# Performance work log

Hardware: AMD Instinct MI355X
Metric: run time of the kernel (lower is better)

Reference implementation:

```python
import jax, jax.numpy as jnp
import numpy as np

E = 1024
B, QL, KVL = 8, 2048, 2048


def setup_inputs() -> dict:
    key = jax.random.key(0)
    ks = jax.random.split(key, 12)
    s = 1.0 / np.sqrt(E)
    return {
        "query": jax.random.normal(ks[0], (B, QL, E), jnp.float32),
        "key_value": jax.random.normal(ks[1], (B, KVL, E), jnp.float32),
        "attention_mask": jax.random.randint(ks[2], (B, QL, KVL), 0, 2, jnp.int32),
        "Wq": jax.random.uniform(ks[3], (E, E), jnp.float32, -s, s),
        "bq": jax.random.uniform(ks[4], (E,), jnp.float32, -s, s),
        "Wk": jax.random.uniform(ks[5], (E, E), jnp.float32, -s, s),
        "bk": jax.random.uniform(ks[6], (E,), jnp.float32, -s, s),
        "Wv": jax.random.uniform(ks[7], (E, E), jnp.float32, -s, s),
        "bv": jax.random.uniform(ks[8], (E,), jnp.float32, -s, s),
        "Wo": jax.random.uniform(ks[9], (E, E), jnp.float32, -s, s),
        "bo": jax.random.uniform(ks[10], (E,), jnp.float32, -s, s),
    }


def reference(query, key_value, attention_mask, Wq, bq, Wk, bk, Wv, bv, Wo, bo):
    # torch Linear: x @ W.T + b
    q = jnp.einsum('bqe,fe->bqf', query, Wq) + bq          # [B, QL, E]
    k = jnp.einsum('bke,fe->bkf', key_value, Wk) + bk      # [B, KVL, E]
    v = jnp.einsum('bke,fe->bkf', key_value, Wv) + bv      # [B, KVL, E]
    scale = 1.0 / jnp.sqrt(jnp.asarray(q.shape[-1], q.dtype))
    attn = jnp.einsum('bqe,bke->bqk', q, k) * scale        # [B, QL, KVL]
    attn = jnp.where(attention_mask == 0, -jnp.inf, attn)
    attn = jax.nn.softmax(attn, axis=-1)
    out = jnp.einsum('bqk,bke->bqe', attn, v)              # [B, QL, E]
    out = jnp.einsum('bqe,fe->bqf', out, Wo) + bo
    return out
```

## Files before the change

### kernel.cpp

```cpp
#include <hip/hip_runtime.h>
#include <hip/hip_bf16.h>
#include <stdint.h>

typedef unsigned short u16;
typedef short s16x8 __attribute__((ext_vector_type(8)));
typedef u16 u16x8 __attribute__((ext_vector_type(8)));
typedef u16 u16x4 __attribute__((ext_vector_type(4)));
typedef float f32x4 __attribute__((ext_vector_type(4)));

__device__ __forceinline__ u16 f2bf(float f) {
  union { float f; uint32_t u; } c; c.f = f;
  uint32_t u = c.u;
  u = u + 0x7fffu + ((u >> 16) & 1u);
  return (u16)(u >> 16);
}
__device__ __forceinline__ float bf2f(u16 b) {
  union { uint32_t u; float f; } c; c.u = ((uint32_t)b) << 16;
  return c.f;
}

__device__ __forceinline__ void gld_lds16(const u16* g, u16* l) {
  __builtin_amdgcn_global_load_lds(
      (const __attribute__((address_space(1))) uint32_t*)g,
      (__attribute__((address_space(3))) uint32_t*)l,
      16, 0, 0);
}

__global__ __launch_bounds__(256) void cvt_f32_to_bf16(
    const float* __restrict__ in, u16* __restrict__ out, long n8) {
  long i = (long)blockIdx.x * blockDim.x + threadIdx.x;
  if (i >= n8) return;
  const float4 a = ((const float4*)in)[i * 2];
  const float4 b = ((const float4*)in)[i * 2 + 1];
  u16x8 r;
  r[0] = f2bf(a.x); r[1] = f2bf(a.y); r[2] = f2bf(a.z); r[3] = f2bf(a.w);
  r[4] = f2bf(b.x); r[5] = f2bf(b.y); r[6] = f2bf(b.z); r[7] = f2bf(b.w);
  *(u16x8*)&out[i * 8] = r;
}

__global__ __launch_bounds__(256) void cvt_w4(
    const float* __restrict__ w0, const float* __restrict__ w1,
    const float* __restrict__ w2, const float* __restrict__ w3,
    u16* __restrict__ out) {
  const float* src = (blockIdx.y == 0) ? w0 : (blockIdx.y == 1) ? w1
                   : (blockIdx.y == 2) ? w2 : w3;
  const long i = (long)blockIdx.x * blockDim.x + threadIdx.x;
  const float4 a = ((const float4*)src)[i * 2];
  const float4 b = ((const float4*)src)[i * 2 + 1];
  u16x8 r;
  r[0] = f2bf(a.x); r[1] = f2bf(a.y); r[2] = f2bf(a.z); r[3] = f2bf(a.w);
  r[4] = f2bf(b.x); r[5] = f2bf(b.y); r[6] = f2bf(b.z); r[7] = f2bf(b.w);
  *(u16x8*)&out[(long)blockIdx.y * 1048576 + i * 8] = r;
}

__global__ __launch_bounds__(256) void transpose64(
    const u16* __restrict__ in, u16* __restrict__ out, int R, int C) {
  __shared__ u16 t[64][66];
  const long ib = (long)blockIdx.z * (long)R * C;
  const int r0 = blockIdx.x * 64, c0 = blockIdx.y * 64;
  const int tid = threadIdx.x;
#pragma unroll
  for (int i = 0; i < 2; ++i) {
    const int ch = i * 256 + tid;
    const int r = ch >> 3, cc = ch & 7;
    const s16x8 v = *(const s16x8*)&in[ib + (long)(r0 + r) * C + c0 + cc * 8];
#pragma unroll
    for (int j = 0; j < 8; ++j) t[r][cc * 8 + j] = (u16)v[j];
  }
  __syncthreads();
#pragma unroll
  for (int i = 0; i < 2; ++i) {
    const int ch = i * 256 + tid;
    const int c = ch >> 3, rr = ch & 7;
    u16x8 r8;
#pragma unroll
    for (int j = 0; j < 8; ++j) r8[j] = t[rr * 8 + j][c];
    *(u16x8*)&out[ib + (long)(c0 + c) * R + r0 + rr * 8] = r8;
  }
}

__global__ __launch_bounds__(256) void bgemv(
    const u16* __restrict__ matA, const float* __restrict__ vecA,
    const u16* __restrict__ matB, const float* __restrict__ vecB,
    const float* __restrict__ addB, float* __restrict__ outA,
    float* __restrict__ outB, float scaleA) {
  __shared__ float w[1024];
  const int tid = threadIdx.x;
  const bool second = blockIdx.x >= 64;
  const u16* mat = second ? matB : matA;
  const float* vec = second ? vecB : vecA;
  const int rb = (second ? (int)blockIdx.x - 64 : (int)blockIdx.x) * 16;
#pragma unroll
  for (int i = 0; i < 4; ++i) w[i * 256 + tid] = vec[i * 256 + tid];
  __syncthreads();
  const int lane = tid & 63, wv_ = tid >> 6;
#pragma unroll
  for (int r = 0; r < 4; ++r) {
    const int row = rb + wv_ * 4 + r;
    const u16* p = &mat[(long)row * 1024 + lane * 16];
    const u16x8 a = *(const u16x8*)p;
    const u16x8 b = *(const u16x8*)(p + 8);
    float s = 0.f;
#pragma unroll
    for (int j = 0; j < 8; ++j) s += bf2f(a[j]) * w[lane * 16 + j];
#pragma unroll
    for (int j = 0; j < 8; ++j) s += bf2f(b[j]) * w[lane * 16 + 8 + j];
#pragma unroll
    for (int off = 32; off >= 1; off >>= 1) s += __shfl_xor(s, off);
    if (lane == 0) {
      if (second) outB[row] = s + addB[row];
      else        outA[row] = s * scaleA;
    }
  }
}

__global__ __launch_bounds__(256) void cgemv(
    const u16* __restrict__ kvbf, const float* __restrict__ wvec,
    float* __restrict__ c) {
  __shared__ float w[1024];
  const int tid = threadIdx.x;
#pragma unroll
  for (int i = 0; i < 4; ++i) w[i * 256 + tid] = wvec[i * 256 + tid];
  __syncthreads();
  const int lane = tid & 63, wv_ = tid >> 6;
  const long rowbase = (long)blockIdx.x * 16 + wv_ * 4;
#pragma unroll
  for (int r = 0; r < 4; ++r) {
    const long row = rowbase + r;
    const u16* p = &kvbf[row * 1024 + lane * 16];
    const u16x8 a = *(const u16x8*)p;
    const u16x8 b = *(const u16x8*)(p + 8);
    float s = 0.f;
#pragma unroll
    for (int j = 0; j < 8; ++j) s += bf2f(a[j]) * w[lane * 16 + j];
#pragma unroll
    for (int j = 0; j < 8; ++j) s += bf2f(b[j]) * w[lane * 16 + 8 + j];
#pragma unroll
    for (int off = 32; off >= 1; off >>= 1) s += __shfl_xor(s, off);
    if (lane == 0) c[row] = s;
  }
}

__global__ __launch_bounds__(256) void softmax_rows(u16* __restrict__ S) {
  const long base = (long)blockIdx.x * 2048;
  const int tid = threadIdx.x;
  const int lane = tid & 63, wave = tid >> 6;
  u16x8 raw = *(const u16x8*)&S[base + tid * 8];
  float v[8];
#pragma unroll
  for (int j = 0; j < 8; ++j) v[j] = bf2f(raw[j]);
  float m = v[0];
#pragma unroll
  for (int j = 1; j < 8; ++j) m = fmaxf(m, v[j]);
#pragma unroll
  for (int off = 32; off >= 1; off >>= 1) m = fmaxf(m, __shfl_xor(m, off));
  __shared__ float red[8];
  if (lane == 0) red[wave] = m;
  __syncthreads();
  m = fmaxf(fmaxf(red[0], red[1]), fmaxf(red[2], red[3]));
  float s = 0.f;
#pragma unroll
  for (int j = 0; j < 8; ++j) { v[j] = __expf(v[j] - m); s += v[j]; }
#pragma unroll
  for (int off = 32; off >= 1; off >>= 1) s += __shfl_xor(s, off);
  if (lane == 0) red[4 + wave] = s;
  __syncthreads();
  s = (red[4] + red[5]) + (red[6] + red[7]);
  const float inv = 1.f / s;
#pragma unroll
  for (int j = 0; j < 8; ++j) raw[j] = f2bf(v[j] * inv);
  *(u16x8*)&S[base + tid * 8] = raw;
}

union __align__(16) SmemT {
  u16 stage[2][128 * 64];
  float epi[32 * 132];
};

__device__ __forceinline__ s16x8 ldsfrag(const u16* p, int r, int c8) {
  return *(const s16x8*)&p[r * 64 + ((c8 ^ (r & 7)) << 3)];
}

__device__ __forceinline__ void stage128(const u16* __restrict__ gb, int row0,
                                         int K, int k0, u16* lbuf, int tid) {
#pragma unroll
  for (int i = 0; i < 4; ++i) {
    const int f = i * 256 + tid;
    const int rl = f >> 3, s = f & 7;
    const int gc = (s ^ (rl & 7)) << 3;
    gld_lds16(gb + (long)(row0 + rl) * K + k0 + gc, lbuf + f * 8);
  }
}

template<bool HAS_BIAS, int MODE, bool HAS_MASK>
__global__ __launch_bounds__(256, 4) void gemm128(
    const u16* __restrict__ A, const u16* __restrict__ B,
    const float* __restrict__ bias, const int* __restrict__ mask,
    void* __restrict__ Cv,
    int M, int N, int K, long sA, long sB, long sC, long sMask, long sBias,
    float scale) {
  __shared__ SmemT sm;
  const int nx = gridDim.x, ny = gridDim.y;
  const int did = blockIdx.x + nx * (blockIdx.y + ny * blockIdx.z);
  const int cpx = (nx * ny * gridDim.z) >> 3;
  const int nf = (did & 7) * cpx + (did >> 3);
  const int b = nf / (nx * ny);
  const int rr = nf % (nx * ny);
  const int bm = (rr / ny) * 128;
  const int bn = (rr % ny) * 128;

  const u16* Ab = A + (long)b * sA;
  const u16* Bb = B + (long)b * sB;
  const float* biasB = HAS_BIAS ? (bias + (long)b * sBias) : nullptr;
  const int tid = threadIdx.x;
  const int lane = tid & 63, wave = tid >> 6;
  const int wm = wave >> 1, wn = wave & 1;
  const int lr = lane & 15, lk = lane >> 4;
  const int NT = K >> 6;

  f32x4 acc[4][4] = {};

  for (int t = 0; t < NT; ++t) {
    stage128(Ab, bm, K, t << 6, sm.stage[0], tid);
    stage128(Bb, bn, K, t << 6, sm.stage[1], tid);
    asm volatile("s_waitcnt vmcnt(0)" ::: "memory");
    __syncthreads();
#pragma unroll
    for (int ks = 0; ks < 2; ++ks) {
      s16x8 af[4], bg[4];
#pragma unroll
      for (int mi = 0; mi < 4; ++mi)
        af[mi] = ldsfrag(sm.stage[0], wm * 64 + mi * 16 + lr, ks * 4 + lk);
#pragma unroll
      for (int ni = 0; ni < 4; ++ni)
        bg[ni] = ldsfrag(sm.stage[1], wn * 64 + ni * 16 + lr, ks * 4 + lk);
#pragma unroll
      for (int mi = 0; mi < 4; ++mi)
#pragma unroll
        for (int ni = 0; ni < 4; ++ni)
          acc[mi][ni] = __builtin_amdgcn_mfma_f32_16x16x32_bf16(
              af[mi], bg[ni], acc[mi][ni], 0, 0, 0);
    }
    __syncthreads();
  }

  const long cb = (long)b * sC;
  const int q = tid & 7, r = tid >> 3;
#pragma unroll
  for (int h = 0; h < 4; ++h) {
    __syncthreads();
    if (wm == (h >> 1)) {
      const int mi0 = (h & 1) * 2;
#pragma unroll
      for (int mm = 0; mm < 2; ++mm) {
        const int mi = mi0 + mm;
#pragma unroll
        for (int ni = 0; ni < 4; ++ni) {
          const int c = wn * 64 + ni * 16 + lr;
          const float bvx = HAS_BIAS ? biasB[bn + c] : 0.f;
#pragma unroll
          for (int j = 0; j < 4; ++j)
            sm.epi[(mm * 16 + (lk << 2) + j) * 132 + c] =
                acc[mi][ni][j] * scale + bvx;
        }
      }
    }
    __syncthreads();
    const int growi = bm + h * 32 + r;
    const long grow = cb + (long)growi * N + bn;
    const long mrow = HAS_MASK
        ? ((long)b * sMask + (long)growi * (long)N + bn) : 0;
#pragma unroll
    for (int ch = 0; ch < 2; ++ch) {
      const int c0 = ch * 64 + q * 8;
      const float4 x = *(const float4*)&sm.epi[r * 132 + c0];
      const float4 y = *(const float4*)&sm.epi[r * 132 + c0 + 4];
      if (MODE == 1) {
        *(float4*)&((float*)Cv)[grow + c0] = x;
        *(float4*)&((float*)Cv)[grow + c0 + 4] = y;
      } else {
        u16x8 pk;
        if (HAS_MASK) {
          const int4 ma = *(const int4*)&mask[mrow + c0];
          const int4 mb = *(const int4*)&mask[mrow + c0 + 4];
          pk[0] = f2bf(ma.x ? x.x : -1e30f);
          pk[1] = f2bf(ma.y ? x.y : -1e30f);
          pk[2] = f2bf(ma.z ? x.z : -1e30f);
          pk[3] = f2bf(ma.w ? x.w : -1e30f);
          pk[4] = f2bf(mb.x ? y.x : -1e30f);
          pk[5] = f2bf(mb.y ? y.y : -1e30f);
          pk[6] = f2bf(mb.z ? y.z : -1e30f);
          pk[7] = f2bf(mb.w ? y.w : -1e30f);
        } else {
          pk[0] = f2bf(x.x); pk[1] = f2bf(x.y);
          pk[2] = f2bf(x.z); pk[3] = f2bf(x.w);
          pk[4] = f2bf(y.x); pk[5] = f2bf(y.y);
          pk[6] = f2bf(y.z); pk[7] = f2bf(y.w);
        }
        *(u16x8*)&((u16*)Cv)[grow + c0] = pk;
      }
    }
  }
}

extern "C" void kernel_launch(void* const* d_in, const int* in_sizes, int n_in,
                              void* d_out, int out_size, void* d_ws, size_t ws_size,
                              hipStream_t stream) {
  const float* query = (const float*)d_in[0];
  const float* kv    = (const float*)d_in[1];
  const int*   mask  = (const int*)d_in[2];
  const float* Wq = (const float*)d_in[3];
  const float* bq = (const float*)d_in[4];
  const float* Wk = (const float*)d_in[5];
  const float* bk = (const float*)d_in[6];
  const float* Wv = (const float*)d_in[7];
  const float* bv = (const float*)d_in[8];
  const float* Wo = (const float*)d_in[9];
  const float* bo = (const float*)d_in[10];
  float* out = (float*)d_out;
  (void)bk;

  char* ws = (char*)d_ws;
  const size_t MB = (size_t)1 << 20;
  u16* qbf  = (u16*)(ws + 0);
  u16* kvbf = (u16*)(ws + 32 * MB);
  u16* wq   = (u16*)(ws + 64 * MB);
  u16* wo   = (u16*)(ws + 70 * MB);
  u16* WqT  = (u16*)(ws + 72 * MB);
  u16* WkT  = (u16*)(ws + 74 * MB);
  u16* Mt   = (u16*)(ws + 78 * MB);
  u16* Wvo  = (u16*)(ws + 80 * MB);
  float* wvec = (float*)(ws + 82 * MB);
  float* bvo  = (float*)(ws + 82 * MB + 65536);
  float* cvec = (float*)(ws + 83 * MB);
  u16* qM   = (u16*)(ws + 84 * MB);
  u16* VwT  = (u16*)(ws + 116 * MB);
  u16* S    = (u16*)(ws + 148 * MB);

  const long sQK = (long)2048 * 1024;
  const long sS  = (long)2048 * 2048;

  cvt_f32_to_bf16<<<8192, 256, 0, stream>>>(query, qbf, 2097152);
  cvt_f32_to_bf16<<<8192, 256, 0, stream>>>(kv, kvbf, 2097152);
  cvt_w4<<<dim3(512, 4, 1), 256, 0, stream>>>(Wq, Wk, Wv, Wo, wq);
  transpose64<<<dim3(16, 16, 3), 256, 0, stream>>>(wq, WqT, 1024, 1024);
  bgemv<<<128, 256, 0, stream>>>(WkT, bq, wo, bv, bo, wvec, bvo, 0.03125f);
  cgemv<<<1024, 256, 0, stream>>>(kvbf, wvec, cvec);

  gemm128<false, 0, false><<<dim3(8, 8, 2), 256, 0, stream>>>(
      WkT, WqT, nullptr, nullptr, Mt, 1024, 1024, 1024,
      -2097152L, 2097152L, 1048576L, 0, 0, 1.f);

  gemm128<false, 0, false><<<dim3(128, 8, 1), 256, 0, stream>>>(
      qbf, Mt, nullptr, nullptr, qM, 16384, 1024, 1024, 0, 0, 0, 0, 0, 1.f);

  gemm128<false, 0, false><<<dim3(8, 16, 8), 256, 0, stream>>>(
      Wvo, kvbf, nullptr, nullptr, VwT, 1024, 2048, 1024,
      0, sQK, sQK, 0, 0, 1.f);

  gemm128<true, 0, true><<<dim3(16, 16, 8), 256, 0, stream>>>(
      qM, kvbf, cvec, mask, S, 2048, 2048, 1024, sQK, sQK, sS, sS, 2048,
      0.03125f);

  softmax_rows<<<16384, 256, 0, stream>>>(S);

  gemm128<true, 1, false><<<dim3(16, 8, 8), 256, 0, stream>>>(
      S, VwT, bvo, nullptr, out, 2048, 1024, 2048, sS, sQK, sQK, 0, 0, 1.f);
}
```

Baseline: 338.1 us.

## Fuse fp32-to-bf16 conversions into transpose, gemv, and GEMM A-tile staging

Merges weight conversion with transposition into a single kernel, fuses the key/value conversion with the c-vector gemv, and drops the separate query conversion by converting fp32 query tiles inside the GEMM's A staging. This removes several launches and intermediate bf16 round trips through memory. The query GEMM now loads fp32 through registers rather than direct-to-LDS async loads, doubling A-side bytes and possibly hurting that GEMM's throughput.

Measured after the change: 351.7 us. 4.0% more time.

```diff
diff --git a/kernel.cpp b/kernel.cpp
--- a/kernel.cpp
+++ b/kernel.cpp
@@ -26,46 +26,40 @@
       16, 0, 0);
 }
 
-__global__ __launch_bounds__(256) void cvt_f32_to_bf16(
-    const float* __restrict__ in, u16* __restrict__ out, long n8) {
-  long i = (long)blockIdx.x * blockDim.x + threadIdx.x;
-  if (i >= n8) return;
-  const float4 a = ((const float4*)in)[i * 2];
-  const float4 b = ((const float4*)in)[i * 2 + 1];
-  u16x8 r;
-  r[0] = f2bf(a.x); r[1] = f2bf(a.y); r[2] = f2bf(a.z); r[3] = f2bf(a.w);
-  r[4] = f2bf(b.x); r[5] = f2bf(b.y); r[6] = f2bf(b.z); r[7] = f2bf(b.w);
-  *(u16x8*)&out[i * 8] = r;
-}
-
-__global__ __launch_bounds__(256) void cvt_w4(
-    const float* __restrict__ w0, const float* __restrict__ w1,
-    const float* __restrict__ w2, const float* __restrict__ w3,
-    u16* __restrict__ out) {
-  const float* src = (blockIdx.y == 0) ? w0 : (blockIdx.y == 1) ? w1
-                   : (blockIdx.y == 2) ? w2 : w3;
-  const long i = (long)blockIdx.x * blockDim.x + threadIdx.x;
-  const float4 a = ((const float4*)src)[i * 2];
-  const float4 b = ((const float4*)src)[i * 2 + 1];
-  u16x8 r;
-  r[0] = f2bf(a.x); r[1] = f2bf(a.y); r[2] = f2bf(a.z); r[3] = f2bf(a.w);
-  r[4] = f2bf(b.x); r[5] = f2bf(b.y); r[6] = f2bf(b.z); r[7] = f2bf(b.w);
-  *(u16x8*)&out[(long)blockIdx.y * 1048576 + i * 8] = r;
-}
-
-__global__ __launch_bounds__(256) void transpose64(
-    const u16* __restrict__ in, u16* __restrict__ out, int R, int C) {
+__global__ __launch_bounds__(256) void cvt_wt(
+    const float* __restrict__ Wq, const float* __restrict__ Wk,
+    const float* __restrict__ Wv, const float* __restrict__ Wo,
+    u16* __restrict__ WqT, u16* __restrict__ WkT, u16* __restrict__ WvT,
+    u16* __restrict__ wo) {
+  const int z = blockIdx.z;
+  const int tid = threadIdx.x;
+  if (z == 3) {
+    const long base = ((long)(blockIdx.y * 16 + blockIdx.x)) * 4096 + tid * 16;
+#pragma unroll
+    for (int h = 0; h < 2; ++h) {
+      const float4 a = *(const float4*)&Wo[base + h * 8];
+      const float4 b = *(const float4*)&Wo[base + h * 8 + 4];
+      u16x8 r;
+      r[0] = f2bf(a.x); r[1] = f2bf(a.y); r[2] = f2bf(a.z); r[3] = f2bf(a.w);
+      r[4] = f2bf(b.x); r[5] = f2bf(b.y); r[6] = f2bf(b.z); r[7] = f2bf(b.w);
+      *(u16x8*)&wo[base + h * 8] = r;
+    }
+    return;
+  }
+  const float* src = (z == 0) ? Wq : (z == 1) ? Wk : Wv;
+  u16* dst = (z == 0) ? WqT : (z == 1) ? WkT : WvT;
   __shared__ u16 t[64][66];
-  const long ib = (long)blockIdx.z * (long)R * C;
   const int r0 = blockIdx.x * 64, c0 = blockIdx.y * 64;
-  const int tid = threadIdx.x;
 #pragma unroll
   for (int i = 0; i < 2; ++i) {
     const int ch = i * 256 + tid;
     const int r = ch >> 3, cc = ch & 7;
-    const s16x8 v = *(const s16x8*)&in[ib + (long)(r0 + r) * C + c0 + cc * 8];
-#pragma unroll
-    for (int j = 0; j < 8; ++j) t[r][cc * 8 + j] = (u16)v[j];
+    const float4 a = *(const float4*)&src[(long)(r0 + r) * 1024 + c0 + cc * 8];
+    const float4 b = *(const float4*)&src[(long)(r0 + r) * 1024 + c0 + cc * 8 + 4];
+    t[r][cc * 8 + 0] = f2bf(a.x); t[r][cc * 8 + 1] = f2bf(a.y);
+    t[r][cc * 8 + 2] = f2bf(a.z); t[r][cc * 8 + 3] = f2bf(a.w);
+    t[r][cc * 8 + 4] = f2bf(b.x); t[r][cc * 8 + 5] = f2bf(b.y);
+    t[r][cc * 8 + 6] = f2bf(b.z); t[r][cc * 8 + 7] = f2bf(b.w);
   }
   __syncthreads();
 #pragma unroll
@@ -75,7 +69,7 @@
     u16x8 r8;
 #pragma unroll
     for (int j = 0; j < 8; ++j) r8[j] = t[rr * 8 + j][c];
-    *(u16x8*)&out[ib + (long)(c0 + c) * R + r0 + rr * 8] = r8;
+    *(u16x8*)&dst[(long)(c0 + c) * 1024 + r0 + rr * 8] = r8;
   }
 }
 
@@ -114,30 +108,38 @@
   }
 }
 
-__global__ __launch_bounds__(256) void cgemv(
-    const u16* __restrict__ kvbf, const float* __restrict__ wvec,
-    float* __restrict__ c) {
+__global__ __launch_bounds__(256) void cvt_kv_c(
+    const float* __restrict__ kv, const float* __restrict__ wvec,
+    u16* __restrict__ kvbf, float* __restrict__ cvec) {
   __shared__ float w[1024];
   const int tid = threadIdx.x;
 #pragma unroll
   for (int i = 0; i < 4; ++i) w[i * 256 + tid] = wvec[i * 256 + tid];
   __syncthreads();
   const int lane = tid & 63, wv_ = tid >> 6;
-  const long rowbase = (long)blockIdx.x * 16 + wv_ * 4;
-#pragma unroll
-  for (int r = 0; r < 4; ++r) {
-    const long row = rowbase + r;
-    const u16* p = &kvbf[row * 1024 + lane * 16];
-    const u16x8 a = *(const u16x8*)p;
-    const u16x8 b = *(const u16x8*)(p + 8);
-    float s = 0.f;
-#pragma unroll
-    for (int j = 0; j < 8; ++j) s += bf2f(a[j]) * w[lane * 16 + j];
-#pragma unroll
-    for (int j = 0; j < 8; ++j) s += bf2f(b[j]) * w[lane * 16 + 8 + j];
+#pragma unroll
+  for (int r = 0; r < 2; ++r) {
+    const long row = (long)blockIdx.x * 8 + wv_ * 2 + r;
+    const float* src = &kv[row * 1024 + lane * 16];
+    const float4 a0 = *(const float4*)src;
+    const float4 a1 = *(const float4*)(src + 4);
+    const float4 a2 = *(const float4*)(src + 8);
+    const float4 a3 = *(const float4*)(src + 12);
+    u16x8 p0, p1;
+    p0[0] = f2bf(a0.x); p0[1] = f2bf(a0.y); p0[2] = f2bf(a0.z); p0[3] = f2bf(a0.w);
+    p0[4] = f2bf(a1.x); p0[5] = f2bf(a1.y); p0[6] = f2bf(a1.z); p0[7] = f2bf(a1.w);
+    p1[0] = f2bf(a2.x); p1[1] = f2bf(a2.y); p1[2] = f2bf(a2.z); p1[3] = f2bf(a2.w);
+    p1[4] = f2bf(a3.x); p1[5] = f2bf(a3.y); p1[6] = f2bf(a3.z); p1[7] = f2bf(a3.w);
+    *(u16x8*)&kvbf[row * 1024 + lane * 16] = p0;
+    *(u16x8*)&kvbf[row * 1024 + lane * 16 + 8] = p1;
+    const float* wl = &w[lane * 16];
+    float s = a0.x * wl[0] + a0.y * wl[1] + a0.z * wl[2] + a0.w * wl[3]
+            + a1.x * wl[4] + a1.y * wl[5] + a1.z * wl[6] + a1.w * wl[7]
+            + a2.x * wl[8] + a2.y * wl[9] + a2.z * wl[10] + a2.w * wl[11]
+            + a3.x * wl[12] + a3.y * wl[13] + a3.z * wl[14] + a3.w * wl[15];
 #pragma unroll
     for (int off = 32; off >= 1; off >>= 1) s += __shfl_xor(s, off);
-    if (lane == 0) c[row] = s;
+    if (lane == 0) cvec[row] = s;
   }
 }
 
@@ -192,9 +194,27 @@
   }
 }
 
-template<bool HAS_BIAS, int MODE, bool HAS_MASK>
+__device__ __forceinline__ void stage128_f32(const float* __restrict__ gb,
+                                             int row0, int K, int k0,
+                                             u16* lbuf, int tid) {
+#pragma unroll
+  for (int i = 0; i < 4; ++i) {
+    const int f = i * 256 + tid;
+    const int rl = f >> 3, s = f & 7;
+    const int gc = (s ^ (rl & 7)) << 3;
+    const float* src = gb + (long)(row0 + rl) * K + k0 + gc;
+    const float4 x = *(const float4*)src;
+    const float4 y = *(const float4*)(src + 4);
+    u16x8 pk;
+    pk[0] = f2bf(x.x); pk[1] = f2bf(x.y); pk[2] = f2bf(x.z); pk[3] = f2bf(x.w);
+    pk[4] = f2bf(y.x); pk[5] = f2bf(y.y); pk[6] = f2bf(y.z); pk[7] = f2bf(y.w);
+    *(u16x8*)&lbuf[f * 8] = pk;
+  }
+}
+
+template<bool HAS_BIAS, int MODE, bool HAS_MASK, int AF32>
 __global__ __launch_bounds__(256, 4) void gemm128(
-    const u16* __restrict__ A, const u16* __restrict__ B,
+    const void* __restrict__ Av, const u16* __restrict__ B,
     const float* __restrict__ bias, const int* __restrict__ mask,
     void* __restrict__ Cv,
     int M, int N, int K, long sA, long sB, long sC, long sMask, long sBias,
@@ -209,7 +229,8 @@
   const int bm = (rr / ny) * 128;
   const int bn = (rr % ny) * 128;
 
-  const u16* Ab = A + (long)b * sA;
+  const u16* Ab16 = AF32 ? nullptr : ((const u16*)Av + (long)b * sA);
+  const float* Abf = AF32 ? ((const float*)Av + (long)b * sA) : nullptr;
   const u16* Bb = B + (long)b * sB;
   const float* biasB = HAS_BIAS ? (bias + (long)b * sBias) : nullptr;
   const int tid = threadIdx.x;
@@ -221,8 +242,9 @@
   f32x4 acc[4][4] = {};
 
   for (int t = 0; t < NT; ++t) {
-    stage128(Ab, bm, K, t << 6, sm.stage[0], tid);
     stage128(Bb, bn, K, t << 6, sm.stage[1], tid);
+    if (AF32) stage128_f32(Abf, bm, K, t << 6, sm.stage[0], tid);
+    else      stage128(Ab16, bm, K, t << 6, sm.stage[0], tid);
     asm volatile("s_waitcnt vmcnt(0)" ::: "memory");
     __syncthreads();
 #pragma unroll
@@ -322,12 +344,11 @@
 
   char* ws = (char*)d_ws;
   const size_t MB = (size_t)1 << 20;
-  u16* qbf  = (u16*)(ws + 0);
   u16* kvbf = (u16*)(ws + 32 * MB);
-  u16* wq   = (u16*)(ws + 64 * MB);
   u16* wo   = (u16*)(ws + 70 * MB);
   u16* WqT  = (u16*)(ws + 72 * MB);
   u16* WkT  = (u16*)(ws + 74 * MB);
+  u16* WvT  = (u16*)(ws + 76 * MB);
   u16* Mt   = (u16*)(ws + 78 * MB);
   u16* Wvo  = (u16*)(ws + 80 * MB);
   float* wvec = (float*)(ws + 82 * MB);
@@ -340,30 +361,29 @@
   const long sQK = (long)2048 * 1024;
   const long sS  = (long)2048 * 2048;
 
-  cvt_f32_to_bf16<<<8192, 256, 0, stream>>>(query, qbf, 2097152);
-  cvt_f32_to_bf16<<<8192, 256, 0, stream>>>(kv, kvbf, 2097152);
-  cvt_w4<<<dim3(512, 4, 1), 256, 0, stream>>>(Wq, Wk, Wv, Wo, wq);
-  transpose64<<<dim3(16, 16, 3), 256, 0, stream>>>(wq, WqT, 1024, 1024);
+  cvt_wt<<<dim3(16, 16, 4), 256, 0, stream>>>(Wq, Wk, Wv, Wo,
+                                              WqT, WkT, WvT, wo);
   bgemv<<<128, 256, 0, stream>>>(WkT, bq, wo, bv, bo, wvec, bvo, 0.03125f);
-  cgemv<<<1024, 256, 0, stream>>>(kvbf, wvec, cvec);
-
-  gemm128<false, 0, false><<<dim3(8, 8, 2), 256, 0, stream>>>(
+
+  cvt_kv_c<<<2048, 256, 0, stream>>>(kv, wvec, kvbf, cvec);
+
+  gemm128<false, 0, false, 0><<<dim3(8, 8, 2), 256, 0, stream>>>(
       WkT, WqT, nullptr, nullptr, Mt, 1024, 1024, 1024,
       -2097152L, 2097152L, 1048576L, 0, 0, 1.f);
 
-  gemm128<false, 0, false><<<dim3(128, 8, 1), 256, 0, stream>>>(
-      qbf, Mt, nullptr, nullptr, qM, 16384, 1024, 1024, 0, 0, 0, 0, 0, 1.f);
-
-  gemm128<false, 0, false><<<dim3(8, 16, 8), 256, 0, stream>>>(
+  gemm128<false, 0, false, 1><<<dim3(128, 8, 1), 256, 0, stream>>>(
+      query, Mt, nullptr, nullptr, qM, 16384, 1024, 1024, 0, 0, 0, 0, 0, 1.f);
+
+  gemm128<false, 0, false, 0><<<dim3(8, 16, 8), 256, 0, stream>>>(
       Wvo, kvbf, nullptr, nullptr, VwT, 1024, 2048, 1024,
       0, sQK, sQK, 0, 0, 1.f);
 
-  gemm128<true, 0, true><<<dim3(16, 16, 8), 256, 0, stream>>>(
+  gemm128<true, 0, true, 0><<<dim3(16, 16, 8), 256, 0, stream>>>(
       qM, kvbf, cvec, mask, S, 2048, 2048, 1024, sQK, sQK, sS, sS, 2048,
       0.03125f);
 
   softmax_rows<<<16384, 256, 0, stream>>>(S);
 
-  gemm128<true, 1, false><<<dim3(16, 8, 8), 256, 0, stream>>>(
+  gemm128<true, 1, false, 0><<<dim3(16, 8, 8), 256, 0, stream>>>(
       S, VwT, bvo, nullptr, out, 2048, 1024, 2048, sS, sQK, sQK, 0, 0, 1.f);
 }
```
